# Kernel tuning notes

Measured on AMD Instinct MI355X. Metric: run time of the kernel, lower is better.

## Reference

```python
import jax, jax.numpy as jnp
import numpy as np
import math

V, D, H, W, P = 256, 512, 8, 128, 6
B, N = 8, 4096
MASK_ID = 1
HEAD_DIM = D // H


def setup_inputs() -> dict:
    key = jax.random.key(0)
    ks = jax.random.split(key, 20)
    s = 0.02
    n = lambda k, shape: jax.random.normal(k, shape, jnp.float32) * s
    return {
        "x": jax.random.randint(ks[0], (B, N), 0, V),
        "mask_ratio_t": jax.random.uniform(ks[1], (B, 1), jnp.float32),
        "tok_emb": n(ks[2], (V, D)),
        "pos_emb": n(ks[3], (8192, D)),
        "mask_emb": n(ks[4], (2, D)),
        "t_W": n(ks[5], (1, D)), "t_b": jnp.zeros((D,), jnp.float32),
        "ln1_s": jnp.ones((D,), jnp.float32), "ln1_b": jnp.zeros((D,), jnp.float32),
        "Wq": n(ks[6], (D, D)), "bq": jnp.zeros((D,), jnp.float32),
        "Wk": n(ks[7], (D, D)), "bk": jnp.zeros((D,), jnp.float32),
        "Wv": n(ks[8], (D, D)), "bv": jnp.zeros((D,), jnp.float32),
        "Wo": n(ks[9], (D, D)), "bo": jnp.zeros((D,), jnp.float32),
        "ln2_s": jnp.ones((D,), jnp.float32), "ln2_b": jnp.zeros((D,), jnp.float32),
        "W1": n(ks[10], (D, 4 * D)), "b1": jnp.zeros((4 * D,), jnp.float32),
        "W2": n(ks[11], (4 * D, D)), "b2": jnp.zeros((D,), jnp.float32),
        "phase_embs": n(ks[12], (P, D)),
        "out_W": n(ks[13], (D, V)), "out_b": jnp.zeros((V,), jnp.float32),
    }


def _layernorm(x, scale, bias, eps=1e-6):
    m = jnp.mean(x, axis=-1, keepdims=True)
    v = jnp.var(x, axis=-1, keepdims=True)
    return (x - m) / jnp.sqrt(v + eps) * scale + bias


def _block(h, ln1_s, ln1_b, Wq, bq, Wk, bk, Wv, bv, Wo, bo, ln2_s, ln2_b, W1, b1, W2, b2):
    # h: (Bw, W, D). Standard pre-LN MHA + MLP; dropout deterministic (identity).
    Bw, Wl, _ = h.shape
    res = h
    x = _layernorm(h, ln1_s, ln1_b)
    q = (x @ Wq + bq).reshape(Bw, Wl, H, HEAD_DIM)
    k = (x @ Wk + bk).reshape(Bw, Wl, H, HEAD_DIM)
    v = (x @ Wv + bv).reshape(Bw, Wl, H, HEAD_DIM)
    attn = jnp.einsum('bihd,bjhd->bhij', q, k) / math.sqrt(HEAD_DIM)
    probs = jax.nn.softmax(attn, axis=-1)
    out = jnp.einsum('bhij,bjhd->bihd', probs, v).reshape(Bw, Wl, D)
    x = out @ Wo + bo + res
    res = x
    y = _layernorm(x, ln2_s, ln2_b)
    y = jax.nn.gelu(y @ W1 + b1) @ W2 + b2
    return y + res


def reference(x, mask_ratio_t, tok_emb, pos_emb, mask_emb, t_W, t_b,
              ln1_s, ln1_b, Wq, bq, Wk, bk, Wv, bv, Wo, bo,
              ln2_s, ln2_b, W1, b1, W2, b2, phase_embs, out_W, out_b):
    Bx, Nx = x.shape
    h = tok_emb[x] + pos_emb[:Nx][None, :, :]
    is_masked = (x == MASK_ID).astype(jnp.int32)
    h = h + mask_emb[is_masked]
    t = jax.nn.gelu(mask_ratio_t @ t_W + t_b)
    h = h + t[:, None, :]
    shift_amt = W // 2
    num_windows = Nx // W
    blk = (ln1_s, ln1_b, Wq, bq, Wk, bk, Wv, bv, Wo, bo, ln2_s, ln2_b, W1, b1, W2, b2)
    for phase in range(P):
        do_shift = (phase % 2 == 1)
        h = h + phase_embs[phase][None, None, :]
        phase_input = h
        if do_shift:
            h = jnp.roll(h, shift=-shift_amt, axis=1)
        hw = h.reshape(Bx * num_windows, W, D)
        hw = _block(hw, *blk)
        h = hw.reshape(Bx, Nx, D)
        if do_shift:
            h = jnp.roll(h, shift=shift_amt, axis=1)
        h = (phase_input + h) * 0.5
    return h @ out_W + out_b
```

## Files before the change

kernel.cpp:

```cpp
#include <hip/hip_runtime.h>
#include <hip/hip_bf16.h>
#include <cstdint>

typedef __bf16 bf16;
typedef __bf16 bf16x8 __attribute__((ext_vector_type(8)));
typedef float f32x4 __attribute__((ext_vector_type(4)));

#define DM 512
#define NTOK 32768

__device__ __forceinline__ float gelu_f(float x) {
  float z = x + 0.044715f * x * x * x;
  return x / (1.f + __expf(-1.5957691216057308f * z));
}

__device__ __forceinline__ void gload_lds16(const bf16* g, bf16* l) {
  __builtin_amdgcn_global_load_lds(
      (const __attribute__((address_space(1))) unsigned int*)g,
      (__attribute__((address_space(3))) unsigned int*)l, 16, 0, 0);
}

__global__ void detect_kernel(const unsigned int* __restrict__ p, int* __restrict__ flag) {
  *flag = (p[0] == 0x3F800000u) ? 0 : 1;
}

__global__ __launch_bounds__(256) void norm_kernel(
    const void* __restrict__ src, bf16* __restrict__ dst, int n,
    const int* __restrict__ flag) {
  int f = *flag;
  int i = (blockIdx.x * 256 + threadIdx.x) * 8;
  int stride = gridDim.x * 2048;
  for (; i < n; i += stride) {
    bf16x8 o;
    if (f == 0) {
      const float* s = (const float*)src;
      float4 a = *(const float4*)(s + i), b = *(const float4*)(s + i + 4);
      o[0] = (bf16)a.x; o[1] = (bf16)a.y; o[2] = (bf16)a.z; o[3] = (bf16)a.w;
      o[4] = (bf16)b.x; o[5] = (bf16)b.y; o[6] = (bf16)b.z; o[7] = (bf16)b.w;
    } else {
      o = *(const bf16x8*)((const bf16*)src + i);
    }
    *(bf16x8*)(dst + i) = o;
  }
}

__global__ __launch_bounds__(256) void transpose_kernel(
    const void* __restrict__ src, bf16* __restrict__ dst, int K, int N,
    const int* __restrict__ flag) {
  __shared__ bf16 tile[32][33];
  int f = *flag;
  int nbx = N >> 5;
  int bx = blockIdx.x % nbx, by = blockIdx.x / nbx;
  int tx = threadIdx.x & 31, ty = threadIdx.x >> 5;
  const float* sf = (const float*)src;
  const bf16* sb = (const bf16*)src;
#pragma unroll
  for (int i = 0; i < 4; i++) {
    int r = by * 32 + ty + i * 8;
    long idx = (long)r * N + bx * 32 + tx;
    tile[ty + i * 8][tx] = (f == 0) ? (bf16)sf[idx] : sb[idx];
  }
  __syncthreads();
#pragma unroll
  for (int i = 0; i < 4; i++) {
    int r = bx * 32 + ty + i * 8;
    dst[(long)r * K + by * 32 + tx] = tile[tx][ty + i * 8];
  }
}

__global__ __launch_bounds__(256) void embed_kernel(
    const int* __restrict__ x, const bf16* __restrict__ mrn,
    const bf16* __restrict__ tok, const bf16* __restrict__ pos,
    const bf16* __restrict__ maske, const bf16* __restrict__ tW,
    const bf16* __restrict__ tb, bf16* __restrict__ h) {
  int t = blockIdx.x * 256 + threadIdx.x;
  int tokid = t >> 6, lane = t & 63;
  int b = tokid >> 12, n = tokid & 4095;
  int xv = x[tokid];
  int d0 = lane * 8;
  bf16x8 te = *(const bf16x8*)(tok + (long)xv * DM + d0);
  bf16x8 pe = *(const bf16x8*)(pos + (long)n * DM + d0);
  bf16x8 me = *(const bf16x8*)(maske + (xv == 1 ? DM : 0) + d0);
  bf16x8 tw = *(const bf16x8*)(tW + d0);
  bf16x8 tbv = *(const bf16x8*)(tb + d0);
  float mrb = (float)mrn[b];
  bf16x8 o;
#pragma unroll
  for (int j = 0; j < 8; j++) {
    float tj = gelu_f(mrb * (float)tw[j] + (float)tbv[j]);
    o[j] = (bf16)((float)te[j] + (float)pe[j] + (float)me[j] + tj);
  }
  *(bf16x8*)(h + (long)tokid * DM + d0) = o;
}

__global__ __launch_bounds__(256) void ln_kernel(
    const bf16* __restrict__ src, bf16* __restrict__ dst,
    const bf16* __restrict__ s, const bf16* __restrict__ bta,
    const bf16* __restrict__ pe, int shift, int tok0) {
  int t = blockIdx.x * 256 + threadIdx.x;
  int tl = t >> 6, lane = t & 63;
  int g = tok0 + tl;
  int b = g >> 12, n = g & 4095;
  long srct = ((long)b << 12) | ((n + shift) & 4095);
  bf16x8 v8 = *(const bf16x8*)(src + srct * DM + lane * 8);
  float vals[8];
  if (pe) {
    bf16x8 p8 = *(const bf16x8*)(pe + lane * 8);
#pragma unroll
    for (int j = 0; j < 8; j++) vals[j] = (float)v8[j] + (float)p8[j];
  } else {
#pragma unroll
    for (int j = 0; j < 8; j++) vals[j] = (float)v8[j];
  }
  float sum = 0.f, sq = 0.f;
#pragma unroll
  for (int j = 0; j < 8; j++) { sum += vals[j]; sq += vals[j] * vals[j]; }
#pragma unroll
  for (int o = 32; o > 0; o >>= 1) {
    sum += __shfl_xor(sum, o);
    sq += __shfl_xor(sq, o);
  }
  float m = sum * (1.f / 512.f);
  float var = sq * (1.f / 512.f) - m * m;
  float r = rsqrtf(var + 1e-6f);
  bf16x8 sv = *(const bf16x8*)(s + lane * 8);
  bf16x8 bv = *(const bf16x8*)(bta + lane * 8);
  bf16x8 o8;
#pragma unroll
  for (int j = 0; j < 8; j++)
    o8[j] = (bf16)(((vals[j] - m) * r) * (float)sv[j] + (float)bv[j]);
  *(bf16x8*)(dst + (long)g * DM + lane * 8) = o8;
}

template <int EPI, int DBUF>
__global__ __launch_bounds__(512) void gemm_kernel(
    const bf16* __restrict__ A, const bf16* __restrict__ Bt,
    const bf16* __restrict__ bias, void* __restrict__ Cv,
    const bf16* __restrict__ res, bf16* __restrict__ hio,
    const bf16* __restrict__ pe,
    int M, int N, int K, int shift, int m0, const int* __restrict__ flag) {
  __shared__ __align__(16) bf16 smem[DBUF ? 32768 : 16384];
  bf16* As = smem;
  bf16* Bs = smem + (DBUF ? 16384 : 8192);
  int tid = threadIdx.x;
  int lane = tid & 63, wv = tid >> 6;
  int wr = wv >> 2, wc = wv & 3;
  int l15 = lane & 15, lk = lane >> 4;
  int ntn = N >> 7;
  int nwg = gridDim.x;
  int q = nwg >> 3, rm = nwg & 7;
  int xcd = blockIdx.x & 7, pos = blockIdx.x >> 3;
  int wgid = (xcd < rm ? xcd * (q + 1) : rm * (q + 1) + (xcd - rm) * q) + pos;
  int mt = wgid / ntn, nt = wgid % ntn;
  const bf16* Abase = A + (long)mt * 128 * K;
  const bf16* Bbase = Bt + (long)nt * 128 * K;
  f32x4 acc[4][2];
#pragma unroll
  for (int i = 0; i < 4; i++)
#pragma unroll
    for (int j = 0; j < 2; j++) acc[i][j] = (f32x4)(0.f);
  int arow0 = wr * 64 + l15;
  int brow0 = wc * 32 + l15;
  int srow[2], scol[2], ldst[2];
#pragma unroll
  for (int r = 0; r < 2; r++) {
    int c2 = r * 512 + tid;
    srow[r] = c2 >> 3;
    scol[r] = ((c2 & 7) ^ (srow[r] & 7)) * 8;
    ldst[r] = c2 * 8;
  }

  if (DBUF) {
    const int nk = K >> 6;
#pragma unroll
    for (int r = 0; r < 2; r++) {
      gload_lds16(Abase + (long)srow[r] * K + scol[r], As + ldst[r]);
      gload_lds16(Bbase + (long)srow[r] * K + scol[r], Bs + ldst[r]);
    }
    __syncthreads();
    for (int t = 0; t < nk; t++) {
      int buf = (t & 1) * 8192;
      int nbuf = 8192 - buf;
      if (t + 1 < nk) {
        const bf16* Ag = Abase + (t + 1) * 64;
        const bf16* Bg = Bbase + (t + 1) * 64;
#pragma unroll
        for (int r = 0; r < 2; r++) {
          gload_lds16(Ag + (long)srow[r] * K + scol[r], As + nbuf + ldst[r]);
          gload_lds16(Bg + (long)srow[r] * K + scol[r], Bs + nbuf + ldst[r]);
        }
      }
#pragma unroll
      for (int kk = 0; kk < 2; kk++) {
        bf16x8 af[4], bfr[2];
#pragma unroll
        for (int i = 0; i < 4; i++) {
          int row = arow0 + i * 16;
          af[i] = *(const bf16x8*)(As + buf + row * 64 + (((kk * 4 + lk) ^ (row & 7)) << 3));
        }
#pragma unroll
        for (int j = 0; j < 2; j++) {
          int row = brow0 + j * 16;
          bfr[j] = *(const bf16x8*)(Bs + buf + row * 64 + (((kk * 4 + lk) ^ (row & 7)) << 3));
        }
#pragma unroll
        for (int i = 0; i < 4; i++)
#pragma unroll
          for (int j = 0; j < 2; j++)
            acc[i][j] = __builtin_amdgcn_mfma_f32_16x16x32_bf16(af[i], bfr[j], acc[i][j], 0, 0, 0);
      }
      __syncthreads();
    }
  } else {
    for (int k0 = 0; k0 < K; k0 += 64) {
#pragma unroll
      for (int r = 0; r < 2; r++) {
        gload_lds16(Abase + (long)srow[r] * K + k0 + scol[r], As + ldst[r]);
        gload_lds16(Bbase + (long)srow[r] * K + k0 + scol[r], Bs + ldst[r]);
      }
      __syncthreads();
#pragma unroll
      for (int kk = 0; kk < 2; kk++) {
        bf16x8 af[4], bfr[2];
#pragma unroll
        for (int i = 0; i < 4; i++) {
          int row = arow0 + i * 16;
          af[i] = *(const bf16x8*)(As + row * 64 + (((kk * 4 + lk) ^ (row & 7)) << 3));
        }
#pragma unroll
        for (int j = 0; j < 2; j++) {
          int row = brow0 + j * 16;
          bfr[j] = *(const bf16x8*)(Bs + row * 64 + (((kk * 4 + lk) ^ (row & 7)) << 3));
        }
#pragma unroll
        for (int i = 0; i < 4; i++)
#pragma unroll
          for (int j = 0; j < 2; j++)
            acc[i][j] = __builtin_amdgcn_mfma_f32_16x16x32_bf16(af[i], bfr[j], acc[i][j], 0, 0, 0);
      }
      __syncthreads();
    }
  }

  int nb0 = nt * 128;
  int lt0 = mt * 128;
  int gt0 = m0 + lt0;
  int bb = gt0 & ~4095, n0 = gt0 & 4095;
  if (EPI == 4) {
    int fl = *flag;
    int mbase = lt0 + wr * 64;
    int nbase = nb0 + wc * 32;
#pragma unroll
    for (int j = 0; j < 2; j++) {
      int col = nbase + j * 16 + l15;
      float bc = (float)bias[col];
#pragma unroll
      for (int i = 0; i < 4; i++) {
        f32x4 a = acc[i][j];
#pragma unroll
        for (int r = 0; r < 4; r++) {
          int mrow = mbase + i * 16 + lk * 4 + r;
          float v = a[r] + bc;
          if (fl == 0) ((float*)Cv)[(long)mrow * N + col] = v;
          else ((bf16*)Cv)[(long)mrow * N + col] = (bf16)v;
        }
      }
    }
    return;
  }

#pragma unroll
  for (int j = 0; j < 2; j++) {
    int lcol = wc * 32 + j * 16 + l15;
    float bc = (float)bias[nb0 + lcol];
    float pc = (EPI == 2 || EPI == 3) ? (float)pe[nb0 + lcol] : 0.f;
#pragma unroll
    for (int i = 0; i < 4; i++) {
      f32x4 a = acc[i][j];
#pragma unroll
      for (int r = 0; r < 4; r++) {
        int lrow = wr * 64 + i * 16 + lk * 4 + r;
        float v = a[r] + bc;
        if (EPI == 1) v = gelu_f(v);
        v += pc;
        smem[lrow * 128 + (lcol ^ ((lrow & 7) << 3))] = (bf16)v;
      }
    }
  }
  __syncthreads();
#pragma unroll
  for (int k = 0; k < 4; k++) {
    int g = k * 512 + tid;
    int row = g >> 4, c16 = g & 15;
    bf16x8 v8 = *(const bf16x8*)(smem + row * 128 + ((c16 ^ (row & 7)) << 3));
    int lt = lt0 + row;
    int gt = gt0 + row;
    int col0 = nb0 + c16 * 8;
    if (EPI == 0 || EPI == 1) {
      *(bf16x8*)((bf16*)Cv + (long)lt * N + col0) = v8;
    } else if (EPI == 2) {
      long srow2 = (long)bb + ((n0 + row + shift) & 4095);
      bf16x8 r8v = *(const bf16x8*)(res + srow2 * DM + col0);
      bf16x8 o;
#pragma unroll
      for (int e = 0; e < 8; e++) o[e] = (bf16)((float)v8[e] + (float)r8v[e]);
      *(bf16x8*)((bf16*)Cv + (long)gt * DM + col0) = o;
    } else {
      bf16x8 r8v = *(const bf16x8*)(res + (long)gt * DM + col0);
      long drow = (long)bb + ((n0 + row + shift) & 4095);
      bf16* hp = hio + drow * DM + col0;
      bf16x8 h8 = *(bf16x8*)hp;
      bf16x8 o;
#pragma unroll
      for (int e = 0; e < 8; e++)
        o[e] = (bf16)(((float)h8[e] + (float)v8[e] + (float)r8v[e]) * 0.5f);
      *(bf16x8*)hp = o;
    }
  }
}

#define LDQ 1536
__device__ __forceinline__ int vt_idx(int d, int kv) {
  return d * 128 + ((((kv >> 3) ^ (d & 15)) & 15) << 3) + (kv & 7);
}
__device__ __forceinline__ int sp_idx(int q, int c) {
  return q * 128 + ((((c >> 3) ^ (q & 15)) & 15) << 3) + (c & 7);
}

__global__ __launch_bounds__(256) void attn_kernel(
    const bf16* __restrict__ QKV, bf16* __restrict__ O) {
  __shared__ __align__(16) bf16 smem[24576];
  bf16* Ks = smem;
  bf16* Vt = smem;
  bf16* SP = smem + 8192;
  int blk = blockIdx.x;
  int w = blk >> 3;
  int hh = blk & 7;
  int tid = threadIdx.x;
  int lane = tid & 63, wv = tid >> 6;
  int l15 = lane & 15, lk = lane >> 4;
  long base = (long)w * 128 * LDQ + hh * 64;
  const bf16* Qg = QKV + base;
  const bf16* Kg = QKV + base + 512;
  const bf16* Vg = QKV + base + 1024;
  int vrow[4], vcol[4];
  bf16x8 vreg[4];
#pragma unroll
  for (int rr = 0; rr < 4; rr++) {
    int c = rr * 256 + tid;
    int row = c >> 3;
    int colc = ((c & 7) ^ (row & 7)) * 8;
    gload_lds16(Kg + (long)row * LDQ + colc, Ks + c * 8);
    vrow[rr] = row;
    vcol[rr] = (c & 7) * 8;
    vreg[rr] = *(const bf16x8*)(Vg + (long)row * LDQ + vcol[rr]);
  }
  __syncthreads();
  f32x4 accs[2][8];
#pragma unroll
  for (int i = 0; i < 2; i++)
#pragma unroll
    for (int j = 0; j < 8; j++) accs[i][j] = (f32x4)(0.f);
#pragma unroll
  for (int ks = 0; ks < 2; ks++) {
    bf16x8 af[2];
#pragma unroll
    for (int im = 0; im < 2; im++)
      af[im] = *(const bf16x8*)(Qg + (long)(wv * 32 + im * 16 + l15) * LDQ + ks * 32 + lk * 8);
#pragma unroll
    for (int in = 0; in < 8; in++) {
      int row = in * 16 + l15;
      bf16x8 bf8 = *(const bf16x8*)(Ks + row * 64 + (((ks * 4 + lk) ^ (row & 7)) << 3));
#pragma unroll
      for (int im = 0; im < 2; im++)
        accs[im][in] = __builtin_amdgcn_mfma_f32_16x16x32_bf16(af[im], bf8, accs[im][in], 0, 0, 0);
    }
  }
  __syncthreads();
#pragma unroll
  for (int rr = 0; rr < 4; rr++) {
#pragma unroll
    for (int j = 0; j < 8; j++) Vt[vt_idx(vcol[rr] + j, vrow[rr])] = vreg[rr][j];
  }
#pragma unroll
  for (int im = 0; im < 2; im++) {
#pragma unroll
    for (int r = 0; r < 4; r++) {
      float mx = accs[im][0][r];
#pragma unroll
      for (int in = 1; in < 8; in++) mx = fmaxf(mx, accs[im][in][r]);
#pragma unroll
      for (int o = 1; o < 16; o <<= 1) mx = fmaxf(mx, __shfl_xor(mx, o));
      float ev[8];
      float sm = 0.f;
#pragma unroll
      for (int in = 0; in < 8; in++) {
        ev[in] = __expf((accs[im][in][r] - mx) * 0.125f);
        sm += ev[in];
      }
#pragma unroll
      for (int o = 1; o < 16; o <<= 1) sm += __shfl_xor(sm, o);
      float inv = 1.f / sm;
#pragma unroll
      for (int in = 0; in < 8; in++) accs[im][in][r] = ev[in] * inv;
    }
  }
#pragma unroll
  for (int im = 0; im < 2; im++)
#pragma unroll
    for (int in = 0; in < 8; in++)
#pragma unroll
      for (int r = 0; r < 4; r++)
        SP[sp_idx(wv * 32 + im * 16 + lk * 4 + r, in * 16 + l15)] =
            (bf16)(accs[im][in][r]);
  __syncthreads();
  f32x4 acco[2][4];
#pragma unroll
  for (int i = 0; i < 2; i++)
#pragma unroll
    for (int j = 0; j < 4; j++) acco[i][j] = (f32x4)(0.f);
#pragma unroll
  for (int ks = 0; ks < 4; ks++) {
    bf16x8 af[2];
#pragma unroll
    for (int im = 0; im < 2; im++) {
      int q = wv * 32 + im * 16 + l15;
      af[im] = *(const bf16x8*)(SP + q * 128 + (((ks * 4 + lk) ^ (q & 15)) << 3));
    }
#pragma unroll
    for (int in = 0; in < 4; in++) {
      int d = in * 16 + l15;
      bf16x8 bf8 = *(const bf16x8*)(Vt + d * 128 + (((ks * 4 + lk) ^ (d & 15)) << 3));
#pragma unroll
      for (int im = 0; im < 2; im++)
        acco[im][in] = __builtin_amdgcn_mfma_f32_16x16x32_bf16(af[im], bf8, acco[im][in], 0, 0, 0);
    }
  }
#pragma unroll
  for (int im = 0; im < 2; im++)
#pragma unroll
    for (int in = 0; in < 4; in++)
#pragma unroll
      for (int r = 0; r < 4; r++)
        O[(long)(w * 128 + wv * 32 + im * 16 + lk * 4 + r) * DM + hh * 64 + in * 16 + l15] =
            (bf16)acco[im][in][r];
}

extern "C" void kernel_launch(void* const* d_in, const int* in_sizes, int n_in,
                              void* d_out, int out_size, void* d_ws, size_t ws_size,
                              hipStream_t stream) {
  (void)in_sizes; (void)n_in; (void)out_size; (void)ws_size;
  const int* x = (const int*)d_in[0];
  const void* mr = d_in[1];
  const void* tok_emb = d_in[2];
  const void* pos_emb = d_in[3];
  const void* mask_emb = d_in[4];
  const void* t_W = d_in[5];
  const void* t_b = d_in[6];
  const void* ln1_s = d_in[7];
  const void* ln1_b = d_in[8];
  const void* Wq = d_in[9];  const void* bq = d_in[10];
  const void* Wk = d_in[11]; const void* bk = d_in[12];
  const void* Wv = d_in[13]; const void* bv = d_in[14];
  const void* Wo = d_in[15]; const void* bo = d_in[16];
  const void* ln2_s = d_in[17]; const void* ln2_b = d_in[18];
  const void* W1 = d_in[19]; const void* b1 = d_in[20];
  const void* W2 = d_in[21]; const void* b2 = d_in[22];
  const void* phase_embs = d_in[23];
  const void* outW = d_in[24]; const void* outb = d_in[25];

  char* ws = (char*)d_ws;
  int* flag = (int*)ws;
  size_t off = 4096;
  auto alloc = [&](size_t bytes) {
    void* p = ws + off;
    off = (off + bytes + 255) & ~(size_t)255;
    return p;
  };
  bf16* mr_n   = (bf16*)alloc(16);
  bf16* tok_n  = (bf16*)alloc(262144);
  bf16* pos_n  = (bf16*)alloc(4194304);
  bf16* mask_n = (bf16*)alloc(2048);
  bf16* tW_n   = (bf16*)alloc(1024);
  bf16* tb_n   = (bf16*)alloc(1024);
  bf16* l1s_n  = (bf16*)alloc(1024);
  bf16* l1b_n  = (bf16*)alloc(1024);
  bf16* l2s_n  = (bf16*)alloc(1024);
  bf16* l2b_n  = (bf16*)alloc(1024);
  bf16* bqkv_n = (bf16*)alloc(3072);
  bf16* bo_n   = (bf16*)alloc(1024);
  bf16* b1_n   = (bf16*)alloc(4096);
  bf16* b2_n   = (bf16*)alloc(1024);
  bf16* ph_n   = (bf16*)alloc(6144);
  bf16* outb_n = (bf16*)alloc(512);
  bf16* WtQKV = (bf16*)alloc(1572864);
  bf16* WtO   = (bf16*)alloc(524288);
  bf16* Wt1   = (bf16*)alloc(2097152);
  bf16* Wt2   = (bf16*)alloc(2097152);
  bf16* WtOut = (bf16*)alloc(262144);
  bf16* h    = (bf16*)(ws + (12ull << 20));
  bf16* x2   = (bf16*)(ws + (44ull << 20));
  bf16* xln  = (bf16*)(ws + (76ull << 20));
  bf16* qkv  = (bf16*)(ws + (108ull << 20));
  bf16* attno = (bf16*)(ws + (204ull << 20));
  bf16* mid  = qkv;

  dim3 blk(256), blk5(512);
  auto ngrid = [](int n) { int g = n / 2048; if (g < 1) g = 1; if (g > 1024) g = 1024; return dim3((unsigned)g); };

  detect_kernel<<<dim3(1), dim3(1), 0, stream>>>((const unsigned int*)ln1_s, flag);

  norm_kernel<<<ngrid(8), blk, 0, stream>>>(mr, mr_n, 8, flag);
  norm_kernel<<<ngrid(131072), blk, 0, stream>>>(tok_emb, tok_n, 131072, flag);
  norm_kernel<<<ngrid(2097152), blk, 0, stream>>>(pos_emb, pos_n, 2097152, flag);
  norm_kernel<<<ngrid(1024), blk, 0, stream>>>(mask_emb, mask_n, 1024, flag);
  norm_kernel<<<ngrid(512), blk, 0, stream>>>(t_W, tW_n, 512, flag);
  norm_kernel<<<ngrid(512), blk, 0, stream>>>(t_b, tb_n, 512, flag);
  norm_kernel<<<ngrid(512), blk, 0, stream>>>(ln1_s, l1s_n, 512, flag);
  norm_kernel<<<ngrid(512), blk, 0, stream>>>(ln1_b, l1b_n, 512, flag);
  norm_kernel<<<ngrid(512), blk, 0, stream>>>(ln2_s, l2s_n, 512, flag);
  norm_kernel<<<ngrid(512), blk, 0, stream>>>(ln2_b, l2b_n, 512, flag);
  norm_kernel<<<ngrid(512), blk, 0, stream>>>(bq, bqkv_n, 512, flag);
  norm_kernel<<<ngrid(512), blk, 0, stream>>>(bk, bqkv_n + 512, 512, flag);
  norm_kernel<<<ngrid(512), blk, 0, stream>>>(bv, bqkv_n + 1024, 512, flag);
  norm_kernel<<<ngrid(512), blk, 0, stream>>>(bo, bo_n, 512, flag);
  norm_kernel<<<ngrid(2048), blk, 0, stream>>>(b1, b1_n, 2048, flag);
  norm_kernel<<<ngrid(512), blk, 0, stream>>>(b2, b2_n, 512, flag);
  norm_kernel<<<ngrid(3072), blk, 0, stream>>>(phase_embs, ph_n, 3072, flag);
  norm_kernel<<<ngrid(256), blk, 0, stream>>>(outb, outb_n, 256, flag);

  transpose_kernel<<<dim3(256), blk, 0, stream>>>(Wq, WtQKV, 512, 512, flag);
  transpose_kernel<<<dim3(256), blk, 0, stream>>>(Wk, WtQKV + 512 * 512, 512, 512, flag);
  transpose_kernel<<<dim3(256), blk, 0, stream>>>(Wv, WtQKV + 1024 * 512, 512, 512, flag);
  transpose_kernel<<<dim3(256), blk, 0, stream>>>(Wo, WtO, 512, 512, flag);
  transpose_kernel<<<dim3(1024), blk, 0, stream>>>(W1, Wt1, 512, 2048, flag);
  transpose_kernel<<<dim3(1024), blk, 0, stream>>>(W2, Wt2, 2048, 512, flag);
  transpose_kernel<<<dim3(128), blk, 0, stream>>>(outW, WtOut, 512, 256, flag);

  embed_kernel<<<dim3(8192), blk, 0, stream>>>(x, mr_n, tok_n, pos_n, mask_n, tW_n, tb_n, h);

  for (int phase = 0; phase < 6; phase++) {
    int shift = (phase & 1) ? 64 : 0;
    const bf16* pe = ph_n + phase * DM;
    ln_kernel<<<dim3(8192), blk, 0, stream>>>(h, xln, l1s_n, l1b_n, pe, shift, 0);
    gemm_kernel<0, 0><<<dim3(256 * 12), blk5, 0, stream>>>(
        xln, WtQKV, bqkv_n, qkv, nullptr, nullptr, nullptr, NTOK, 1536, 512, 0, 0, flag);
    attn_kernel<<<dim3(2048), blk, 0, stream>>>(qkv, attno);
    gemm_kernel<2, 0><<<dim3(256 * 4), blk5, 0, stream>>>(
        attno, WtO, bo_n, x2, h, nullptr, pe, NTOK, 512, 512, shift, 0, flag);
    for (int c = 0; c < 2; c++) {
      int m0 = c * 16384;
      ln_kernel<<<dim3(4096), blk, 0, stream>>>(x2, xln, l2s_n, l2b_n, nullptr, 0, m0);
      gemm_kernel<1, 0><<<dim3(128 * 16), blk5, 0, stream>>>(
          xln + (long)m0 * DM, Wt1, b1_n, mid, nullptr, nullptr, nullptr,
          16384, 2048, 512, 0, m0, flag);
      gemm_kernel<3, 1><<<dim3(128 * 4), blk5, 0, stream>>>(
          mid, Wt2, b2_n, nullptr, x2, h, pe, 16384, 512, 2048, shift, m0, flag);
    }
  }

  gemm_kernel<4, 0><<<dim3(256 * 2), blk5, 0, stream>>>(
      h, WtOut, outb_n, d_out, nullptr, nullptr, nullptr, NTOK, 256, 512, 0, 0, flag);
}
```

Measured before the change: 2.023 ms.

## Fold LayerNorm into GEMMs via per-token stats and precomputed weight vectors

```diff
diff --git a/kernel.cpp b/kernel.cpp
--- a/kernel.cpp
+++ b/kernel.cpp
@@ -46,7 +46,7 @@
 
 __global__ __launch_bounds__(256) void transpose_kernel(
     const void* __restrict__ src, bf16* __restrict__ dst, int K, int N,
-    const int* __restrict__ flag) {
+    const int* __restrict__ flag, const bf16* __restrict__ scale) {
   __shared__ bf16 tile[32][33];
   int f = *flag;
   int nbx = N >> 5;
@@ -58,7 +58,9 @@
   for (int i = 0; i < 4; i++) {
     int r = by * 32 + ty + i * 8;
     long idx = (long)r * N + bx * 32 + tx;
-    tile[ty + i * 8][tx] = (f == 0) ? (bf16)sf[idx] : sb[idx];
+    float wv = (f == 0) ? sf[idx] : (float)sb[idx];
+    if (scale) wv *= (float)scale[r];
+    tile[ty + i * 8][tx] = (bf16)wv;
   }
   __syncthreads();
 #pragma unroll
@@ -66,6 +68,42 @@
     int r = bx * 32 + ty + i * 8;
     dst[(long)r * K + by * 32 + tx] = tile[tx][ty + i * 8];
   }
+}
+
+__global__ void prep_kernel(const bf16* __restrict__ s1, const bf16* __restrict__ b1l,
+                            const bf16* __restrict__ s2, const bf16* __restrict__ b2l,
+                            const bf16* __restrict__ ph, bf16* __restrict__ va) {
+  int d = threadIdx.x;
+  va[d] = s1[d];
+  va[512 + d] = b1l[d];
+#pragma unroll
+  for (int p = 0; p < 6; p++)
+    va[(2 + p) * 512 + d] = (bf16)((float)s1[d] * (float)ph[p * 512 + d]);
+  va[8 * 512 + d] = s2[d];
+  va[9 * 512 + d] = b2l[d];
+}
+
+__global__ __launch_bounds__(256) void gemv_kernel(
+    const void* __restrict__ Wa, const void* __restrict__ Wb, const void* __restrict__ Wc,
+    const bf16* __restrict__ va_buf, const bf16* __restrict__ bias,
+    float* __restrict__ u_out, float* __restrict__ c_out, float* __restrict__ pw_out,
+    int Ntot, int wwidth, const int* __restrict__ flag) {
+  int f = *flag;
+  int chunks = Ntot >> 8;
+  int v = blockIdx.x / chunks, ch = blockIdx.x % chunks;
+  int n = ch * 256 + threadIdx.x;
+  int arr = n / wwidth, nl = n % wwidth;
+  const void* W = (arr == 0) ? Wa : (arr == 1 ? Wb : Wc);
+  const bf16* va = va_buf + v * 512;
+  float acc = 0.f;
+  for (int d = 0; d < 512; d++) {
+    float w = (f == 0) ? ((const float*)W)[(long)d * wwidth + nl]
+                       : (float)((const bf16*)W)[(long)d * wwidth + nl];
+    acc += (float)va[d] * w;
+  }
+  if (v == 0) u_out[n] = acc;
+  else if (v == 1) c_out[n] = acc + (float)bias[n];
+  else pw_out[(v - 2) * Ntot + n] = acc;
 }
 
 __global__ __launch_bounds__(256) void embed_kernel(
@@ -93,16 +131,13 @@
   *(bf16x8*)(h + (long)tokid * DM + d0) = o;
 }
 
-__global__ __launch_bounds__(256) void ln_kernel(
-    const bf16* __restrict__ src, bf16* __restrict__ dst,
-    const bf16* __restrict__ s, const bf16* __restrict__ bta,
-    const bf16* __restrict__ pe, int shift, int tok0) {
+__global__ __launch_bounds__(256) void stats_kernel(
+    const bf16* __restrict__ src, const bf16* __restrict__ pe,
+    float2* __restrict__ out, int tok0) {
   int t = blockIdx.x * 256 + threadIdx.x;
-  int tl = t >> 6, lane = t & 63;
-  int g = tok0 + tl;
-  int b = g >> 12, n = g & 4095;
-  long srct = ((long)b << 12) | ((n + shift) & 4095);
-  bf16x8 v8 = *(const bf16x8*)(src + srct * DM + lane * 8);
+  int tok = tok0 + (t >> 6);
+  int lane = t & 63;
+  bf16x8 v8 = *(const bf16x8*)(src + (long)tok * DM + lane * 8);
   float vals[8];
   if (pe) {
     bf16x8 p8 = *(const bf16x8*)(pe + lane * 8);
@@ -123,13 +158,7 @@
   float m = sum * (1.f / 512.f);
   float var = sq * (1.f / 512.f) - m * m;
   float r = rsqrtf(var + 1e-6f);
-  bf16x8 sv = *(const bf16x8*)(s + lane * 8);
-  bf16x8 bv = *(const bf16x8*)(bta + lane * 8);
-  bf16x8 o8;
-#pragma unroll
-  for (int j = 0; j < 8; j++)
-    o8[j] = (bf16)(((vals[j] - m) * r) * (float)sv[j] + (float)bv[j]);
-  *(bf16x8*)(dst + (long)g * DM + lane * 8) = o8;
+  if (lane == 0) out[tok] = make_float2(r, m * r);
 }
 
 template <int EPI, int DBUF>
@@ -138,6 +167,8 @@
     const bf16* __restrict__ bias, void* __restrict__ Cv,
     const bf16* __restrict__ res, bf16* __restrict__ hio,
     const bf16* __restrict__ pe,
+    const float2* __restrict__ stats, const float* __restrict__ uvec,
+    const float* __restrict__ cvec, const float* __restrict__ pwvec,
     int M, int N, int K, int shift, int m0, const int* __restrict__ flag) {
   __shared__ __align__(16) bf16 smem[DBUF ? 32768 : 16384];
   bf16* As = smem;
@@ -152,7 +183,9 @@
   int xcd = blockIdx.x & 7, pos = blockIdx.x >> 3;
   int wgid = (xcd < rm ? xcd * (q + 1) : rm * (q + 1) + (xcd - rm) * q) + pos;
   int mt = wgid / ntn, nt = wgid % ntn;
-  const bf16* Abase = A + (long)mt * 128 * K;
+  int lt0 = mt * 128;
+  int gt0 = m0 + lt0;
+  int bb = gt0 & ~4095, n0 = gt0 & 4095;
   const bf16* Bbase = Bt + (long)nt * 128 * K;
   f32x4 acc[4][2];
 #pragma unroll
@@ -161,33 +194,37 @@
     for (int j = 0; j < 2; j++) acc[i][j] = (f32x4)(0.f);
   int arow0 = wr * 64 + l15;
   int brow0 = wc * 32 + l15;
-  int srow[2], scol[2], ldst[2];
+  long aoff[2], boff[2];
+  int ldst[2];
 #pragma unroll
   for (int r = 0; r < 2; r++) {
     int c2 = r * 512 + tid;
-    srow[r] = c2 >> 3;
-    scol[r] = ((c2 & 7) ^ (srow[r] & 7)) * 8;
+    int srow = c2 >> 3;
+    int scol = ((c2 & 7) ^ (srow & 7)) * 8;
+    long grow = (EPI == 5) ? ((long)bb + ((n0 + srow + shift) & 4095))
+                           : ((long)lt0 + srow);
+    aoff[r] = grow * K + scol;
+    boff[r] = (long)srow * K + scol;
     ldst[r] = c2 * 8;
   }
+  const bf16* Ab0 = (EPI == 5) ? A : A;
 
   if (DBUF) {
     const int nk = K >> 6;
 #pragma unroll
     for (int r = 0; r < 2; r++) {
-      gload_lds16(Abase + (long)srow[r] * K + scol[r], As + ldst[r]);
-      gload_lds16(Bbase + (long)srow[r] * K + scol[r], Bs + ldst[r]);
+      gload_lds16(Ab0 + aoff[r], As + ldst[r]);
+      gload_lds16(Bbase + boff[r], Bs + ldst[r]);
     }
     __syncthreads();
     for (int t = 0; t < nk; t++) {
       int buf = (t & 1) * 8192;
       int nbuf = 8192 - buf;
       if (t + 1 < nk) {
-        const bf16* Ag = Abase + (t + 1) * 64;
-        const bf16* Bg = Bbase + (t + 1) * 64;
 #pragma unroll
         for (int r = 0; r < 2; r++) {
-          gload_lds16(Ag + (long)srow[r] * K + scol[r], As + nbuf + ldst[r]);
-          gload_lds16(Bg + (long)srow[r] * K + scol[r], Bs + nbuf + ldst[r]);
+          gload_lds16(Ab0 + aoff[r] + (t + 1) * 64, As + nbuf + ldst[r]);
+          gload_lds16(Bbase + boff[r] + (t + 1) * 64, Bs + nbuf + ldst[r]);
         }
       }
 #pragma unroll
@@ -215,8 +252,8 @@
     for (int k0 = 0; k0 < K; k0 += 64) {
 #pragma unroll
       for (int r = 0; r < 2; r++) {
-        gload_lds16(Abase + (long)srow[r] * K + k0 + scol[r], As + ldst[r]);
-        gload_lds16(Bbase + (long)srow[r] * K + k0 + scol[r], Bs + ldst[r]);
+        gload_lds16(Ab0 + aoff[r] + k0, As + ldst[r]);
+        gload_lds16(Bbase + boff[r] + k0, Bs + ldst[r]);
       }
       __syncthreads();
 #pragma unroll
@@ -243,9 +280,6 @@
   }
 
   int nb0 = nt * 128;
-  int lt0 = mt * 128;
-  int gt0 = m0 + lt0;
-  int bb = gt0 & ~4095, n0 = gt0 & 4095;
   if (EPI == 4) {
     int fl = *flag;
     int mbase = lt0 + wr * 64;
@@ -269,21 +303,47 @@
     return;
   }
 
-#pragma unroll
-  for (int j = 0; j < 2; j++) {
-    int lcol = wc * 32 + j * 16 + l15;
-    float bc = (float)bias[nb0 + lcol];
-    float pc = (EPI == 2 || EPI == 3) ? (float)pe[nb0 + lcol] : 0.f;
+  if (EPI == 5 || EPI == 6) {
+    float fu[2], fc[2], fp[2];
+#pragma unroll
+    for (int j = 0; j < 2; j++) {
+      int col = nb0 + wc * 32 + j * 16 + l15;
+      fu[j] = uvec[col];
+      fc[j] = cvec[col];
+      fp[j] = (EPI == 5) ? pwvec[col] : 0.f;
+    }
 #pragma unroll
     for (int i = 0; i < 4; i++) {
-      f32x4 a = acc[i][j];
 #pragma unroll
       for (int r = 0; r < 4; r++) {
         int lrow = wr * 64 + i * 16 + lk * 4 + r;
-        float v = a[r] + bc;
-        if (EPI == 1) v = gelu_f(v);
-        v += pc;
-        smem[lrow * 128 + (lcol ^ ((lrow & 7) << 3))] = (bf16)v;
+        long sig = (EPI == 5) ? ((long)bb + ((n0 + lrow + shift) & 4095))
+                              : ((long)gt0 + lrow);
+        float2 st = stats[sig];
+#pragma unroll
+        for (int j = 0; j < 2; j++) {
+          int lcol = wc * 32 + j * 16 + l15;
+          float v;
+          if (EPI == 5) v = st.x * (acc[i][j][r] + fp[j]) - st.y * fu[j] + fc[j];
+          else          v = gelu_f(st.x * acc[i][j][r] - st.y * fu[j] + fc[j]);
+          smem[lrow * 128 + (lcol ^ ((lrow & 7) << 3))] = (bf16)v;
+        }
+      }
+    }
+  } else {
+#pragma unroll
+    for (int j = 0; j < 2; j++) {
+      int lcol = wc * 32 + j * 16 + l15;
+      float bc = (float)bias[nb0 + lcol];
+      float pc = (float)pe[nb0 + lcol];
+#pragma unroll
+      for (int i = 0; i < 4; i++) {
+        f32x4 a = acc[i][j];
+#pragma unroll
+        for (int r = 0; r < 4; r++) {
+          int lrow = wr * 64 + i * 16 + lk * 4 + r;
+          smem[lrow * 128 + (lcol ^ ((lrow & 7) << 3))] = (bf16)(a[r] + bc + pc);
+        }
       }
     }
   }
@@ -296,7 +356,7 @@
     int lt = lt0 + row;
     int gt = gt0 + row;
     int col0 = nb0 + c16 * 8;
-    if (EPI == 0 || EPI == 1) {
+    if (EPI == 5 || EPI == 6) {
       *(bf16x8*)((bf16*)Cv + (long)lt * N + col0) = v8;
     } else if (EPI == 2) {
       long srow2 = (long)bb + ((n0 + row + shift) & 4095);
@@ -498,9 +558,16 @@
   bf16* Wt1   = (bf16*)alloc(2097152);
   bf16* Wt2   = (bf16*)alloc(2097152);
   bf16* WtOut = (bf16*)alloc(262144);
+  bf16*  va_buf = (bf16*)alloc(10240);
+  float* u_qkv  = (float*)alloc(6144);
+  float* c_qkv  = (float*)alloc(6144);
+  float* pw_qkv = (float*)alloc(36864);
+  float* u_1    = (float*)alloc(8192);
+  float* c_1    = (float*)alloc(8192);
+  float2* stats1 = (float2*)alloc(262144);
+  float2* stats2 = (float2*)alloc(262144);
   bf16* h    = (bf16*)(ws + (12ull << 20));
   bf16* x2   = (bf16*)(ws + (44ull << 20));
-  bf16* xln  = (bf16*)(ws + (76ull << 20));
   bf16* qkv  = (bf16*)(ws + (108ull << 20));
   bf16* attno = (bf16*)(ws + (204ull << 20));
   bf16* mid  = qkv;
@@ -529,36 +596,46 @@
   norm_kernel<<<ngrid(3072), blk, 0, stream>>>(phase_embs, ph_n, 3072, flag);
   norm_kernel<<<ngrid(256), blk, 0, stream>>>(outb, outb_n, 256, flag);
 
-  transpose_kernel<<<dim3(256), blk, 0, stream>>>(Wq, WtQKV, 512, 512, flag);
-  transpose_kernel<<<dim3(256), blk, 0, stream>>>(Wk, WtQKV + 512 * 512, 512, 512, flag);
-  transpose_kernel<<<dim3(256), blk, 0, stream>>>(Wv, WtQKV + 1024 * 512, 512, 512, flag);
-  transpose_kernel<<<dim3(256), blk, 0, stream>>>(Wo, WtO, 512, 512, flag);
-  transpose_kernel<<<dim3(1024), blk, 0, stream>>>(W1, Wt1, 512, 2048, flag);
-  transpose_kernel<<<dim3(1024), blk, 0, stream>>>(W2, Wt2, 2048, 512, flag);
-  transpose_kernel<<<dim3(128), blk, 0, stream>>>(outW, WtOut, 512, 256, flag);
+  transpose_kernel<<<dim3(256), blk, 0, stream>>>(Wq, WtQKV, 512, 512, flag, l1s_n);
+  transpose_kernel<<<dim3(256), blk, 0, stream>>>(Wk, WtQKV + 512 * 512, 512, 512, flag, l1s_n);
+  transpose_kernel<<<dim3(256), blk, 0, stream>>>(Wv, WtQKV + 1024 * 512, 512, 512, flag, l1s_n);
+  transpose_kernel<<<dim3(256), blk, 0, stream>>>(Wo, WtO, 512, 512, flag, nullptr);
+  transpose_kernel<<<dim3(1024), blk, 0, stream>>>(W1, Wt1, 512, 2048, flag, l2s_n);
+  transpose_kernel<<<dim3(1024), blk, 0, stream>>>(W2, Wt2, 2048, 512, flag, nullptr);
+  transpose_kernel<<<dim3(128), blk, 0, stream>>>(outW, WtOut, 512, 256, flag, nullptr);
+
+  prep_kernel<<<dim3(1), dim3(512), 0, stream>>>(l1s_n, l1b_n, l2s_n, l2b_n, ph_n, va_buf);
+  gemv_kernel<<<dim3(48), blk, 0, stream>>>(Wq, Wk, Wv, va_buf, bqkv_n,
+                                            u_qkv, c_qkv, pw_qkv, 1536, 512, flag);
+  gemv_kernel<<<dim3(16), blk, 0, stream>>>(W1, W1, W1, va_buf + 8 * 512, b1_n,
+                                            u_1, c_1, nullptr, 2048, 2048, flag);
 
   embed_kernel<<<dim3(8192), blk, 0, stream>>>(x, mr_n, tok_n, pos_n, mask_n, tW_n, tb_n, h);
 
   for (int phase = 0; phase < 6; phase++) {
     int shift = (phase & 1) ? 64 : 0;
     const bf16* pe = ph_n + phase * DM;
-    ln_kernel<<<dim3(8192), blk, 0, stream>>>(h, xln, l1s_n, l1b_n, pe, shift, 0);
-    gemm_kernel<0, 0><<<dim3(256 * 12), blk5, 0, stream>>>(
-        xln, WtQKV, bqkv_n, qkv, nullptr, nullptr, nullptr, NTOK, 1536, 512, 0, 0, flag);
+    stats_kernel<<<dim3(8192), blk, 0, stream>>>(h, pe, stats1, 0);
+    gemm_kernel<5, 0><<<dim3(256 * 12), blk5, 0, stream>>>(
+        h, WtQKV, nullptr, qkv, nullptr, nullptr, nullptr,
+        stats1, u_qkv, c_qkv, pw_qkv + phase * 1536, NTOK, 1536, 512, shift, 0, flag);
     attn_kernel<<<dim3(2048), blk, 0, stream>>>(qkv, attno);
     gemm_kernel<2, 0><<<dim3(256 * 4), blk5, 0, stream>>>(
-        attno, WtO, bo_n, x2, h, nullptr, pe, NTOK, 512, 512, shift, 0, flag);
+        attno, WtO, bo_n, x2, h, nullptr, pe,
+        nullptr, nullptr, nullptr, nullptr, NTOK, 512, 512, shift, 0, flag);
     for (int c = 0; c < 2; c++) {
       int m0 = c * 16384;
-      ln_kernel<<<dim3(4096), blk, 0, stream>>>(x2, xln, l2s_n, l2b_n, nullptr, 0, m0);
-      gemm_kernel<1, 0><<<dim3(128 * 16), blk5, 0, stream>>>(
-          xln + (long)m0 * DM, Wt1, b1_n, mid, nullptr, nullptr, nullptr,
-          16384, 2048, 512, 0, m0, flag);
+      stats_kernel<<<dim3(4096), blk, 0, stream>>>(x2, nullptr, stats2, m0);
+      gemm_kernel<6, 0><<<dim3(128 * 16), blk5, 0, stream>>>(
+          x2 + (long)m0 * DM, Wt1, nullptr, mid, nullptr, nullptr, nullptr,
+          stats2, u_1, c_1, nullptr, 16384, 2048, 512, 0, m0, flag);
       gemm_kernel<3, 1><<<dim3(128 * 4), blk5, 0, stream>>>(
-          mid, Wt2, b2_n, nullptr, x2, h, pe, 16384, 512, 2048, shift, m0, flag);
+          mid, Wt2, b2_n, nullptr, x2, h, pe,
+          nullptr, nullptr, nullptr, nullptr, 16384, 512, 2048, shift, m0, flag);
     }
   }
 
   gemm_kernel<4, 0><<<dim3(256 * 2), blk5, 0, stream>>>(
-      h, WtOut, outb_n, d_out, nullptr, nullptr, nullptr, NTOK, 256, 512, 0, 0, flag);
-}
+      h, WtOut, outb_n, d_out, nullptr, nullptr, nullptr,
+      nullptr, nullptr, nullptr, nullptr, NTOK, 256, 512, 0, 0, flag);
+}
```

Result: slower. 2.088 ms (+3.2%).
